# Kernel optimization log

Hardware: AMD Instinct MI355X
Metric: run time of the kernel (lower is better)

The kernel has to match this reference:

```python
import jax, jax.numpy as jnp
import numpy as np

N_HEADS = 16
NEG_INF = -10000.0


def setup_inputs() -> dict:
    key = jax.random.key(0)
    k1, k2, k3, k4 = jax.random.split(key, 4)
    B, S, D = 2, 2048, 1024
    q = jax.random.normal(k1, (B, S, D), dtype=jnp.float32)
    k = jax.random.normal(k2, (B, S, D), dtype=jnp.float32)
    v = jax.random.normal(k3, (B, S, D), dtype=jnp.float32)
    mask = jax.random.randint(k4, (B, S, S), 0, 2, dtype=jnp.int32)
    return {"q": q, "k": k, "v": v, "mask": mask}


def _mha(q, k, v, mask):
    B, S, D = q.shape
    H = N_HEADS
    hd = D // H
    # [B,S,D] -> [B,H,S,hd]
    qh = q.reshape(B, S, H, hd).transpose(0, 2, 1, 3)
    kh = k.reshape(B, S, H, hd).transpose(0, 2, 1, 3)
    vh = v.reshape(B, S, H, hd).transpose(0, 2, 1, 3)
    scores = jnp.einsum('bhqd,bhkd->bhqk', qh, kh) / jnp.sqrt(jnp.float32(hd))
    scores = scores + mask[:, None, :, :].astype(scores.dtype) * NEG_INF
    probs = jax.nn.softmax(scores, axis=-1)
    out = jnp.einsum('bhqk,bhkd->bhqd', probs, vh)
    return out.transpose(0, 2, 1, 3).reshape(B, S, D)


def reference(q, k, v, mask):
    return _mha(q, k, v, mask)
```

## Files before the change

kernel.cpp:

```cpp
#include <hip/hip_runtime.h>
#include <stdint.h>

#define S_LEN 2048
#define DMODEL 1024
#define NH 16
#define HD 64
#define NWORDS (S_LEN / 32)
#define NT (S_LEN / 64)

typedef __attribute__((ext_vector_type(4))) float f32x4;
typedef __attribute__((ext_vector_type(8))) short s16x8;
typedef __attribute__((ext_vector_type(4))) short s16x4;
typedef __attribute__((ext_vector_type(4))) int i32x4;
typedef __attribute__((ext_vector_type(2))) uint32_t u32x2;

__device__ __forceinline__ short f2bf(float x) {
  union { float f; uint32_t u; } v; v.f = x;
  return (short)((v.u + 0x8000u) >> 16);
}

__device__ __forceinline__ uint32_t cvtpk(float a, float b) {
  uint32_t r;
  asm("v_cvt_pk_bf16_f32 %0, %1, %2" : "=v"(r) : "v"(a), "v"(b));
  return r;
}

__device__ __forceinline__ float hexp2(float x) {
#if __has_builtin(__builtin_amdgcn_exp2f)
  return __builtin_amdgcn_exp2f(x);
#else
  float r;
  asm("v_exp_f32 %0, %1" : "=v"(r) : "v"(x));
  return r;
#endif
}

__device__ __forceinline__ f32x4 mfma32(s16x8 a, s16x8 b, f32x4 c) {
  return __builtin_amdgcn_mfma_f32_16x16x32_bf16(a, b, c, 0, 0, 0);
}

__device__ __forceinline__ f32x4 mfma16(s16x4 a, s16x4 b, f32x4 c) {
#if __has_builtin(__builtin_amdgcn_mfma_f32_16x16x16bf16_1k)
  return __builtin_amdgcn_mfma_f32_16x16x16bf16_1k(a, b, c, 0, 0, 0);
#else
  f32x4 d;
  asm("v_mfma_f32_16x16x16_bf16 %0, %1, %2, %3" : "=&v"(d) : "v"(a), "v"(b), "v"(c));
  return d;
#endif
}

typedef const __attribute__((address_space(1))) uint32_t* gas_u32p;
typedef __attribute__((address_space(3))) uint32_t* las_u32p;
__device__ __forceinline__ void gl_lds16(const void* g, void* l) {
  __builtin_amdgcn_global_load_lds((gas_u32p)g, (las_u32p)l, 16, 0, 0);
}

__global__ __launch_bounds__(256) void maskpack_kernel(
    const int* __restrict__ mask, uint32_t* __restrict__ bits, int ngroups) {
  const int lane = threadIdx.x & 63;
  const int wave = blockIdx.x * (blockDim.x >> 6) + (threadIdx.x >> 6);
  const int nw = gridDim.x * (blockDim.x >> 6);
  for (int gi = wave; gi < ngroups; gi += nw) {
    const int m = mask[(size_t)gi * 64 + lane];
    const unsigned long long bal = __ballot(m != 0);
    if (lane == 0) {
      bits[(size_t)gi * 2]     = (uint32_t)bal;
      bits[(size_t)gi * 2 + 1] = (uint32_t)(bal >> 32);
    }
  }
}

__global__ __launch_bounds__(256) void packkv_kernel(
    const float* __restrict__ k, const float* __restrict__ v,
    short* __restrict__ Kp, short* __restrict__ Vp) {
  const int t = blockIdx.x, h = blockIdx.y;
  const int b = blockIdx.z & 1, which = blockIdx.z >> 1;
  if (which == 0) {
    short* dst = Kp + (((size_t)(b * NH + h) * NT) + t) * 4096;
    const float* src0 = k + ((size_t)b * S_LEN + t * 64) * DMODEL + h * HD;
    for (int c = threadIdx.x; c < 512; c += 256) {
      const int kv = c >> 3, j = c & 7;
      const int jsrc = j ^ (kv & 7);
      const float* p = src0 + (size_t)kv * DMODEL + jsrc * 8;
      const f32x4 a = *(const f32x4*)p;
      const f32x4 bb = *(const f32x4*)(p + 4);
      s16x8 o;
      o[0]=f2bf(a[0]);  o[1]=f2bf(a[1]);  o[2]=f2bf(a[2]);  o[3]=f2bf(a[3]);
      o[4]=f2bf(bb[0]); o[5]=f2bf(bb[1]); o[6]=f2bf(bb[2]); o[7]=f2bf(bb[3]);
      *(s16x8*)(dst + (size_t)c * 8) = o;
    }
  } else {
    short* dst = Vp + (((size_t)(b * NH + h) * NT) + t) * 4096;
    const float* src0 = v + ((size_t)b * S_LEN + t * 64) * DMODEL + h * HD;
    for (int c = threadIdx.x; c < 1024; c += 256) {
      const int quad = c >> 6, dd = c & 63;
      const int d = dd ^ (quad & 7);
      const float* p = src0 + (size_t)quad * 4 * DMODEL + d;
      s16x4 o;
      o[0] = f2bf(p[0]);
      o[1] = f2bf(p[DMODEL]);
      o[2] = f2bf(p[2 * DMODEL]);
      o[3] = f2bf(p[3 * DMODEL]);
      *(s16x4*)(dst + (size_t)c * 4) = o;
    }
  }
}

__device__ __forceinline__ void tile_step7(
    int buf,
    const char*& kg, const char*& vg,
    const uint32_t*& bp0, const uint32_t*& bp1,
    char* klsb, char* vlsb, int so,
    int ka0, int ka1, int voE, int voO, int g4,
    const s16x8& qf00, const s16x8& qf01,
    const s16x8& qf10, const s16x8& qf11,
    u32x2& mwn0, u32x2& mwn1,
    f32x4 acc0[4], f32x4 acc1[4], f32x4& accs0, f32x4& accs1) {
  const f32x4 z4 = {0.f, 0.f, 0.f, 0.f};

  const u32x2 mw0 = mwn0, mw1 = mwn1;
  mwn0 = *(const u32x2*)bp0; bp0 += 2;
  mwn1 = *(const u32x2*)bp1; bp1 += 2;

  {
    char* kl = klsb + (buf ^ 1) * 8192 + so;
    char* vl = vlsb + (buf ^ 1) * 8192 + so;
    gl_lds16(kg, kl);  gl_lds16(kg + 1024, kl + 1024);
    gl_lds16(vg, vl);  gl_lds16(vg + 1024, vl + 1024);
    kg += 8192;
    vg += 8192;
  }

  f32x4 st0[4], st1[4];
  __builtin_amdgcn_s_setprio(1);
#pragma unroll
  for (int mi = 0; mi < 4; ++mi) {
    const char* rp = klsb + buf * 8192 + mi * 2048;
    const s16x8 kf0 = *(const s16x8*)(rp + ka0);
    const s16x8 kf1 = *(const s16x8*)(rp + ka1);
    st0[mi] = mfma32(kf1, qf01, mfma32(kf0, qf00, z4));
    st1[mi] = mfma32(kf1, qf11, mfma32(kf0, qf10, z4));
  }
  __builtin_amdgcn_s_setprio(0);

  const uint32_t wlo0 = mw0[0] >> g4, whi0 = mw0[1] >> g4;
  const uint32_t wlo1 = mw1[0] >> g4, whi1 = mw1[1] >> g4;
  s16x4 pf0[4], pf1[4];
#pragma unroll
  for (int mi = 0; mi < 4; ++mi) {
    const uint32_t w0 = (mi < 2) ? wlo0 : whi0;
    const uint32_t w1 = (mi < 2) ? wlo1 : whi1;
    const int bpos = (mi & 1) << 4;
    float p0[4], p1[4];
#pragma unroll
    for (int r = 0; r < 4; ++r) {
      union { float f; uint32_t u; } a, c;
      a.f = hexp2(st0[mi][r]);
      a.u &= (((w0 >> (bpos + r)) & 1u) - 1u);
      p0[r] = a.f;
      c.f = hexp2(st1[mi][r]);
      c.u &= (((w1 >> (bpos + r)) & 1u) - 1u);
      p1[r] = c.f;
    }
    union { uint32_t u[2]; s16x4 v4; } k0, k1;
    k0.u[0] = cvtpk(p0[0], p0[1]);  k0.u[1] = cvtpk(p0[2], p0[3]);
    k1.u[0] = cvtpk(p1[0], p1[1]);  k1.u[1] = cvtpk(p1[2], p1[3]);
    pf0[mi] = k0.v4;
    pf1[mi] = k1.v4;
  }

  const s16x4 onesb = {(short)0x3F80, (short)0x3F80, (short)0x3F80, (short)0x3F80};
  __builtin_amdgcn_s_setprio(1);
#pragma unroll
  for (int kc = 0; kc < 4; ++kc) {
    const char* vb = vlsb + buf * 8192 + kc * 2048;
    const int vo = (kc & 1) ? voO : voE;
    accs0 = mfma16(pf0[kc], onesb, accs0);
    accs1 = mfma16(pf1[kc], onesb, accs1);
#pragma unroll
    for (int dt = 0; dt < 4; ++dt) {
      const s16x4 vf = *(const s16x4*)(vb + dt * 128 + vo);
      acc0[dt] = mfma16(pf0[kc], vf, acc0[dt]);
      acc1[dt] = mfma16(pf1[kc], vf, acc1[dt]);
    }
  }
  __builtin_amdgcn_s_setprio(0);

  asm volatile("s_waitcnt vmcnt(0)" ::: "memory");
  __syncthreads();
}

__global__ __launch_bounds__(256, 2) void attn7_kernel(
    const float* __restrict__ q, const char* __restrict__ Kp,
    const char* __restrict__ Vp, const uint32_t* __restrict__ bits,
    float* __restrict__ out) {
  const int tid = threadIdx.x, lane = tid & 63, wid = tid >> 6;
  const int lq = lane & 15, g = lane >> 4, g4 = g << 2;

  const int wg = blockIdx.x;
  const int sz = ((wg & 7) << 6) | (wg >> 3);
  const int bx = sz & 15;
  const int h  = (sz >> 4) & 15;
  const int b  = sz >> 8;

  const int qbase = bx * 128 + wid * 32;
  const size_t bS = (size_t)b * S_LEN;
  const int qr0 = qbase + lq;
  const int qr1 = qbase + 16 + lq;

  __shared__ __align__(16) short kls[2][4096];
  __shared__ __align__(16) short vls[2][4096];

  const f32x4 z4 = {0.f, 0.f, 0.f, 0.f};
  const float SC = 0.125f * 1.44269504088896f;

  s16x8 qf00, qf01, qf10, qf11;
  {
    const float* qp = q + (bS + qr0) * (size_t)DMODEL + h * HD + g * 8;
    const f32x4 a0 = *(const f32x4*)qp;
    const f32x4 a1 = *(const f32x4*)(qp + 4);
    const f32x4 b0 = *(const f32x4*)(qp + 32);
    const f32x4 b1 = *(const f32x4*)(qp + 36);
    qf00[0]=f2bf(a0[0]*SC); qf00[1]=f2bf(a0[1]*SC);
    qf00[2]=f2bf(a0[2]*SC); qf00[3]=f2bf(a0[3]*SC);
    qf00[4]=f2bf(a1[0]*SC); qf00[5]=f2bf(a1[1]*SC);
    qf00[6]=f2bf(a1[2]*SC); qf00[7]=f2bf(a1[3]*SC);
    qf01[0]=f2bf(b0[0]*SC); qf01[1]=f2bf(b0[1]*SC);
    qf01[2]=f2bf(b0[2]*SC); qf01[3]=f2bf(b0[3]*SC);
    qf01[4]=f2bf(b1[0]*SC); qf01[5]=f2bf(b1[1]*SC);
    qf01[6]=f2bf(b1[2]*SC); qf01[7]=f2bf(b1[3]*SC);
  }
  {
    const float* qp = q + (bS + qr1) * (size_t)DMODEL + h * HD + g * 8;
    const f32x4 a0 = *(const f32x4*)qp;
    const f32x4 a1 = *(const f32x4*)(qp + 4);
    const f32x4 b0 = *(const f32x4*)(qp + 32);
    const f32x4 b1 = *(const f32x4*)(qp + 36);
    qf10[0]=f2bf(a0[0]*SC); qf10[1]=f2bf(a0[1]*SC);
    qf10[2]=f2bf(a0[2]*SC); qf10[3]=f2bf(a0[3]*SC);
    qf10[4]=f2bf(a1[0]*SC); qf10[5]=f2bf(a1[1]*SC);
    qf10[6]=f2bf(a1[2]*SC); qf10[7]=f2bf(a1[3]*SC);
    qf11[0]=f2bf(b0[0]*SC); qf11[1]=f2bf(b0[1]*SC);
    qf11[2]=f2bf(b0[2]*SC); qf11[3]=f2bf(b0[3]*SC);
    qf11[4]=f2bf(b1[0]*SC); qf11[5]=f2bf(b1[1]*SC);
    qf11[6]=f2bf(b1[2]*SC); qf11[7]=f2bf(b1[3]*SC);
  }

  const char* kg = Kp + ((size_t)(b * NH + h) * NT) * 8192 + wid * 2048 + lane * 16;
  const char* vg = Vp + ((size_t)(b * NH + h) * NT) * 8192 + wid * 2048 + lane * 16;
  const uint32_t* bp0 = bits + (bS + qr0) * NWORDS;
  const uint32_t* bp1 = bits + (bS + qr1) * NWORDS;

  f32x4 acc0[4] = {z4, z4, z4, z4};
  f32x4 acc1[4] = {z4, z4, z4, z4};
  f32x4 accs0 = z4, accs1 = z4;

  const int swk = (lq & 7) << 4;
  const int ka0 = lq * 128 + ((g * 16) ^ swk);
  const int ka1 = lq * 128 + ((64 + g * 16) ^ swk);
  const int voE = g * 512 + ((lq * 8) ^ (g * 8));
  const int voO = g * 512 + ((lq * 8) ^ (g * 8 + 32));
  const int so  = wid * 2048;

  u32x2 mwn0 = *(const u32x2*)bp0;  bp0 += 2;
  u32x2 mwn1 = *(const u32x2*)bp1;  bp1 += 2;

  {
    char* kl = (char*)kls + so;
    char* vl = (char*)vls + so;
    gl_lds16(kg, kl);  gl_lds16(kg + 1024, kl + 1024);
    gl_lds16(vg, vl);  gl_lds16(vg + 1024, vl + 1024);
    kg += 8192; vg += 8192;
  }
  asm volatile("s_waitcnt vmcnt(0)" ::: "memory");
  __syncthreads();

  for (int t2 = 0; t2 < NT; t2 += 2) {
    tile_step7(0, kg, vg, bp0, bp1, (char*)kls, (char*)vls, so,
               ka0, ka1, voE, voO, g4, qf00, qf01, qf10, qf11,
               mwn0, mwn1, acc0, acc1, accs0, accs1);
    tile_step7(1, kg, vg, bp0, bp1, (char*)kls, (char*)vls, so,
               ka0, ka1, voE, voO, g4, qf00, qf01, qf10, qf11,
               mwn0, mwn1, acc0, acc1, accs0, accs1);
  }

  float li0[4], li1[4];
#pragma unroll
  for (int r = 0; r < 4; ++r) {
    li0[r] = 1.0f / fmaxf(accs0[r], 1e-30f);
    li1[r] = 1.0f / fmaxf(accs1[r], 1e-30f);
  }
  float* ob0 = out + (bS + qbase) * (size_t)DMODEL + h * HD;
  float* ob1 = ob0 + (size_t)16 * DMODEL;
#pragma unroll
  for (int dt = 0; dt < 4; ++dt)
#pragma unroll
    for (int r = 0; r < 4; ++r) {
      ob0[(size_t)(g4 + r) * DMODEL + dt * 16 + lq] = acc0[dt][r] * li0[r];
      ob1[(size_t)(g4 + r) * DMODEL + dt * 16 + lq] = acc1[dt][r] * li1[r];
    }
}

template <int MASKBITS>
__global__ __launch_bounds__(256) void attn_kernel(
    const float* __restrict__ q, const float* __restrict__ k,
    const float* __restrict__ v, const int* __restrict__ mask,
    const uint32_t* __restrict__ bits, float* __restrict__ out) {
  const int tid  = threadIdx.x;
  const int lane = tid & 63;
  const int wid  = tid >> 6;
  const int lq   = lane & 15;
  const int g    = lane >> 4;
  const int g4   = g << 2;
  const int b    = blockIdx.z;
  const int h    = blockIdx.y;
  const int qw   = blockIdx.x * 128 + wid * 32;

  __shared__ __align__(16) short kls[64 * 64];
  __shared__ __align__(16) short vls[64 * 64];

  const size_t bS = (size_t)b * S_LEN;
  const float* qbase = q + bS * DMODEL + h * HD;
  const float* kbase = k + bS * DMODEL + h * HD;
  const float* vbase = v + bS * DMODEL + h * HD;

  const float LOG2E = 1.44269504088896f;
  const f32x4 z4 = {0.f, 0.f, 0.f, 0.f};

  s16x8 qf[2][2];
#pragma unroll
  for (int nq = 0; nq < 2; ++nq)
#pragma unroll
    for (int dc = 0; dc < 2; ++dc) {
      const float* p = qbase + (size_t)(qw + nq * 16 + lq) * DMODEL + dc * 32 + g * 8;
      const f32x4 a = *(const f32x4*)p;
      const f32x4 c = *(const f32x4*)(p + 4);
      s16x8 f;
      f[0] = f2bf(a[0] * 0.125f); f[1] = f2bf(a[1] * 0.125f);
      f[2] = f2bf(a[2] * 0.125f); f[3] = f2bf(a[3] * 0.125f);
      f[4] = f2bf(c[0] * 0.125f); f[5] = f2bf(c[1] * 0.125f);
      f[6] = f2bf(c[2] * 0.125f); f[7] = f2bf(c[3] * 0.125f);
      qf[nq][dc] = f;
    }

  f32x4 acc[2][4];
#pragma unroll
  for (int nq = 0; nq < 2; ++nq)
#pragma unroll
    for (int dt = 0; dt < 4; ++dt) acc[nq][dt] = z4;
  float mrun[2] = {-3.0e38f, -3.0e38f};
  float lrun[2] = {0.f, 0.f};

  const int kr  = tid >> 2;
  const int kc4 = (tid & 3) * 16;
  const int vq  = tid >> 4;
  const int vd  = (tid & 15) * 4;

  for (int t = 0; t < NT; ++t) {
    const int kvb = t * 64;
    uint32_t mw0[2], mw1[2];
    i32x4 mdir[2][4];
    if (MASKBITS) {
#pragma unroll
      for (int nq = 0; nq < 2; ++nq) {
        const uint32_t* bpp = bits + (bS + qw + nq * 16 + lq) * NWORDS + (kvb >> 5);
        const u32x2 w = *(const u32x2*)bpp;
        mw0[nq] = w[0]; mw1[nq] = w[1];
      }
    } else {
#pragma unroll
      for (int nq = 0; nq < 2; ++nq)
#pragma unroll
        for (int mi = 0; mi < 4; ++mi)
          mdir[nq][mi] = *(const i32x4*)(mask + (bS + qw + nq * 16 + lq) * S_LEN +
                                         kvb + mi * 16 + g4);
    }

    __syncthreads();
    {
      const float* p = kbase + (size_t)(kvb + kr) * DMODEL + kc4;
      const f32x4 x0 = *(const f32x4*)p;
      const f32x4 x1 = *(const f32x4*)(p + 4);
      const f32x4 x2 = *(const f32x4*)(p + 8);
      const f32x4 x3 = *(const f32x4*)(p + 12);
      s16x8 lo, hi;
      lo[0]=f2bf(x0[0]); lo[1]=f2bf(x0[1]); lo[2]=f2bf(x0[2]); lo[3]=f2bf(x0[3]);
      lo[4]=f2bf(x1[0]); lo[5]=f2bf(x1[1]); lo[6]=f2bf(x1[2]); lo[7]=f2bf(x1[3]);
      hi[0]=f2bf(x2[0]); hi[1]=f2bf(x2[1]); hi[2]=f2bf(x2[2]); hi[3]=f2bf(x2[3]);
      hi[4]=f2bf(x3[0]); hi[5]=f2bf(x3[1]); hi[6]=f2bf(x3[2]); hi[7]=f2bf(x3[3]);
      char* rowp = (char*)kls + kr * 128;
      const int sw2 = (kr & 7) << 4;
      *(s16x8*)(rowp + ((kc4 * 2) ^ sw2))      = lo;
      *(s16x8*)(rowp + ((kc4 * 2 + 16) ^ sw2)) = hi;
    }
    {
      const float* p = vbase + (size_t)(kvb + vq * 4) * DMODEL + vd;
      const f32x4 r0 = *(const f32x4*)p;
      const f32x4 r1 = *(const f32x4*)(p + DMODEL);
      const f32x4 r2 = *(const f32x4*)(p + 2 * DMODEL);
      const f32x4 r3 = *(const f32x4*)(p + 3 * DMODEL);
      char* rowp = (char*)vls + vq * 512;
      const int sw2 = (vq & 7) << 3;
#pragma unroll
      for (int j = 0; j < 4; ++j) {
        s16x4 pk;
        pk[0] = f2bf(r0[j]); pk[1] = f2bf(r1[j]);
        pk[2] = f2bf(r2[j]); pk[3] = f2bf(r3[j]);
        *(s16x4*)(rowp + (((vd + j) * 8) ^ sw2)) = pk;
      }
    }
    __syncthreads();

    f32x4 stv[2][4];
#pragma unroll
    for (int mi = 0; mi < 4; ++mi) {
      const char* rp = (const char*)kls + (mi * 16 + lq) * 128;
      const int sw2 = (lq & 7) << 4;
      const s16x8 kf0 = *(const s16x8*)(rp + ((g * 16) ^ sw2));
      const s16x8 kf1 = *(const s16x8*)(rp + ((64 + g * 16) ^ sw2));
      stv[0][mi] = mfma32(kf0, qf[0][0], z4);
      stv[0][mi] = mfma32(kf1, qf[0][1], stv[0][mi]);
      stv[1][mi] = mfma32(kf0, qf[1][0], z4);
      stv[1][mi] = mfma32(kf1, qf[1][1], stv[1][mi]);
    }

    s16x4 pf[2][4];
#pragma unroll
    for (int nq = 0; nq < 2; ++nq) {
#pragma unroll
      for (int mi = 0; mi < 4; ++mi) {
#pragma unroll
        for (int r = 0; r < 4; ++r) {
          float mz;
          if (MASKBITS) {
            const uint32_t w = (mi < 2) ? mw0[nq] : mw1[nq];
            const int sh = ((mi & 1) << 4) + g4 + r;
            mz = (float)((w >> sh) & 1u);
          } else {
            mz = (float)mdir[nq][mi][r];
          }
          stv[nq][mi][r] = stv[nq][mi][r] - 10000.0f * mz;
        }
      }
      float mx = -3.0e38f;
#pragma unroll
      for (int mi = 0; mi < 4; ++mi)
#pragma unroll
        for (int r = 0; r < 4; ++r) mx = fmaxf(mx, stv[nq][mi][r]);
      mx = fmaxf(mx, __shfl_xor(mx, 16));
      mx = fmaxf(mx, __shfl_xor(mx, 32));
      const float mnew = fmaxf(mrun[nq], mx);
      const float al = exp2f((mrun[nq] - mnew) * LOG2E);
      mrun[nq] = mnew;
      const float nms = mnew * LOG2E;
      float sum = 0.f;
#pragma unroll
      for (int mi = 0; mi < 4; ++mi)
#pragma unroll
        for (int r = 0; r < 4; ++r) {
          const float p = exp2f(__builtin_fmaf(stv[nq][mi][r], LOG2E, -nms));
          stv[nq][mi][r] = p;
          sum += p;
        }
      sum += __shfl_xor(sum, 16);
      sum += __shfl_xor(sum, 32);
      lrun[nq] = lrun[nq] * al + sum;
      float aO[4];
#pragma unroll
      for (int r = 0; r < 4; ++r) aO[r] = __shfl(al, g4 + r);
#pragma unroll
      for (int dt = 0; dt < 4; ++dt)
#pragma unroll
        for (int r = 0; r < 4; ++r) acc[nq][dt][r] *= aO[r];
#pragma unroll
      for (int kc = 0; kc < 4; ++kc) {
        s16x4 pp;
#pragma unroll
        for (int r = 0; r < 4; ++r) pp[r] = f2bf(stv[nq][kc][r]);
        pf[nq][kc] = pp;
      }
    }

#pragma unroll
    for (int kc = 0; kc < 4; ++kc) {
#pragma unroll
      for (int dt = 0; dt < 4; ++dt) {
        const int quad = kc * 4 + g;
        const s16x4 vf = *(const s16x4*)((const char*)vls + quad * 512 +
                                         (((dt * 16 + lq) * 8) ^ ((quad & 7) << 3)));
        acc[0][dt] = mfma16(pf[0][kc], vf, acc[0][dt]);
        acc[1][dt] = mfma16(pf[1][kc], vf, acc[1][dt]);
      }
    }
  }

  float* obase = out + bS * DMODEL + h * HD;
#pragma unroll
  for (int nq = 0; nq < 2; ++nq) {
    const float linv = 1.0f / lrun[nq];
    float li[4];
#pragma unroll
    for (int r = 0; r < 4; ++r) li[r] = __shfl(linv, g4 + r);
#pragma unroll
    for (int dt = 0; dt < 4; ++dt)
#pragma unroll
      for (int r = 0; r < 4; ++r)
        obase[(size_t)(qw + nq * 16 + g4 + r) * DMODEL + dt * 16 + lq] =
            acc[nq][dt][r] * li[r];
  }
}

extern "C" void kernel_launch(void* const* d_in, const int* in_sizes, int n_in,
                              void* d_out, int out_size, void* d_ws, size_t ws_size,
                              hipStream_t stream) {
  const float* q   = (const float*)d_in[0];
  const float* k   = (const float*)d_in[1];
  const float* v   = (const float*)d_in[2];
  const int* mask  = (const int*)d_in[3];
  float* out       = (float*)d_out;

  const size_t bits_bytes = (size_t)2 * S_LEN * NWORDS * sizeof(uint32_t);
  const size_t pack_bytes = (size_t)2 * S_LEN * DMODEL * sizeof(short);
  const size_t full_bytes = bits_bytes + 2 * pack_bytes + 16384;

  if (ws_size >= full_bytes) {
    char* w = (char*)d_ws;
    uint32_t* bits = (uint32_t*)w;
    char* Kp = w + bits_bytes;
    char* Vp = w + bits_bytes + pack_bytes;

    const int ngroups = 2 * S_LEN * (S_LEN / 64);
    maskpack_kernel<<<512, 256, 0, stream>>>(mask, bits, ngroups);
    packkv_kernel<<<dim3(NT, NH, 4), 256, 0, stream>>>(k, v, (short*)Kp, (short*)Vp);
    attn7_kernel<<<512, 256, 0, stream>>>(q, Kp, Vp, bits, out);
  } else if (ws_size >= bits_bytes) {
    uint32_t* bits = (uint32_t*)d_ws;
    const int ngroups = 2 * S_LEN * (S_LEN / 64);
    maskpack_kernel<<<512, 256, 0, stream>>>(mask, bits, ngroups);
    attn_kernel<1><<<dim3(S_LEN / 128, NH, 2), 256, 0, stream>>>(
        q, k, v, mask, bits, out);
  } else {
    attn_kernel<0><<<dim3(S_LEN / 128, NH, 2), 256, 0, stream>>>(
        q, k, v, mask, nullptr, out);
  }
}
```

Measured before the change: 93.55 us.

## Split KV sequence across two wave groups per block with LDS reduction

Doubles the block to 512 threads, with two groups of four waves each handling half of the key/value tiles (16 tiles each) for the same 128 query rows. Each group has its own double-buffered K/V LDS region. Partial output and row-sum accumulators are then combined through shared memory before normalization and store. This aims to shorten the serial KV loop per block and raise the number of waves in flight. The cost is more LDS per block (64KB), an extra reduction and barrier, and possible occupancy limits at 512 threads.

Result: no change. 95.25 us (+1.8%).

```diff
diff --git a/kernel.cpp b/kernel.cpp
--- a/kernel.cpp
+++ b/kernel.cpp
@@ -190,11 +190,12 @@
   __syncthreads();
 }
 
-__global__ __launch_bounds__(256, 2) void attn7_kernel(
+__global__ __launch_bounds__(512, 2) void attn8_kernel(
     const float* __restrict__ q, const char* __restrict__ Kp,
     const char* __restrict__ Vp, const uint32_t* __restrict__ bits,
     float* __restrict__ out) {
   const int tid = threadIdx.x, lane = tid & 63, wid = tid >> 6;
+  const int qw4 = wid & 3, ks = wid >> 2;
   const int lq = lane & 15, g = lane >> 4, g4 = g << 2;
 
   const int wg = blockIdx.x;
@@ -203,13 +204,14 @@
   const int h  = (sz >> 4) & 15;
   const int b  = sz >> 8;
 
-  const int qbase = bx * 128 + wid * 32;
+  const int qbase = bx * 128 + qw4 * 32;
   const size_t bS = (size_t)b * S_LEN;
   const int qr0 = qbase + lq;
   const int qr1 = qbase + 16 + lq;
 
-  __shared__ __align__(16) short kls[2][4096];
-  __shared__ __align__(16) short vls[2][4096];
+  __shared__ __align__(16) char smem[65536];
+  char* klsb = smem + ks * 16384;
+  char* vlsb = smem + 32768 + ks * 16384;
 
   const f32x4 z4 = {0.f, 0.f, 0.f, 0.f};
   const float SC = 0.125f * 1.44269504088896f;
@@ -246,10 +248,12 @@
     qf11[6]=f2bf(b1[2]*SC); qf11[7]=f2bf(b1[3]*SC);
   }
 
-  const char* kg = Kp + ((size_t)(b * NH + h) * NT) * 8192 + wid * 2048 + lane * 16;
-  const char* vg = Vp + ((size_t)(b * NH + h) * NT) * 8192 + wid * 2048 + lane * 16;
-  const uint32_t* bp0 = bits + (bS + qr0) * NWORDS;
-  const uint32_t* bp1 = bits + (bS + qr1) * NWORDS;
+  const char* kg = Kp + ((size_t)(b * NH + h) * NT + ks * 16) * 8192 +
+                   qw4 * 2048 + lane * 16;
+  const char* vg = Vp + ((size_t)(b * NH + h) * NT + ks * 16) * 8192 +
+                   qw4 * 2048 + lane * 16;
+  const uint32_t* bp0 = bits + (bS + qr0) * NWORDS + ks * 32;
+  const uint32_t* bp1 = bits + (bS + qr1) * NWORDS + ks * 32;
 
   f32x4 acc0[4] = {z4, z4, z4, z4};
   f32x4 acc1[4] = {z4, z4, z4, z4};
@@ -260,14 +264,14 @@
   const int ka1 = lq * 128 + ((64 + g * 16) ^ swk);
   const int voE = g * 512 + ((lq * 8) ^ (g * 8));
   const int voO = g * 512 + ((lq * 8) ^ (g * 8 + 32));
-  const int so  = wid * 2048;
+  const int so  = qw4 * 2048;
 
   u32x2 mwn0 = *(const u32x2*)bp0;  bp0 += 2;
   u32x2 mwn1 = *(const u32x2*)bp1;  bp1 += 2;
 
   {
-    char* kl = (char*)kls + so;
-    char* vl = (char*)vls + so;
+    char* kl = klsb + so;
+    char* vl = vlsb + so;
     gl_lds16(kg, kl);  gl_lds16(kg + 1024, kl + 1024);
     gl_lds16(vg, vl);  gl_lds16(vg + 1024, vl + 1024);
     kg += 8192; vg += 8192;
@@ -275,30 +279,53 @@
   asm volatile("s_waitcnt vmcnt(0)" ::: "memory");
   __syncthreads();
 
-  for (int t2 = 0; t2 < NT; t2 += 2) {
-    tile_step7(0, kg, vg, bp0, bp1, (char*)kls, (char*)vls, so,
+  for (int t2 = 0; t2 < 16; t2 += 2) {
+    tile_step7(0, kg, vg, bp0, bp1, klsb, vlsb, so,
                ka0, ka1, voE, voO, g4, qf00, qf01, qf10, qf11,
                mwn0, mwn1, acc0, acc1, accs0, accs1);
-    tile_step7(1, kg, vg, bp0, bp1, (char*)kls, (char*)vls, so,
+    tile_step7(1, kg, vg, bp0, bp1, klsb, vlsb, so,
                ka0, ka1, voE, voO, g4, qf00, qf01, qf10, qf11,
                mwn0, mwn1, acc0, acc1, accs0, accs1);
   }
 
-  float li0[4], li1[4];
-#pragma unroll
-  for (int r = 0; r < 4; ++r) {
-    li0[r] = 1.0f / fmaxf(accs0[r], 1e-30f);
-    li1[r] = 1.0f / fmaxf(accs1[r], 1e-30f);
-  }
-  float* ob0 = out + (bS + qbase) * (size_t)DMODEL + h * HD;
-  float* ob1 = ob0 + (size_t)16 * DMODEL;
-#pragma unroll
-  for (int dt = 0; dt < 4; ++dt)
+  float* red = (float*)smem;
+  if (ks == 1) {
+    float* rp = red + (size_t)(qw4 * 64 + lane) * 44;
+#pragma unroll
+    for (int dt = 0; dt < 4; ++dt) {
+      *(f32x4*)(rp + 4 * dt)      = acc0[dt];
+      *(f32x4*)(rp + 16 + 4 * dt) = acc1[dt];
+    }
+    *(f32x4*)(rp + 32) = accs0;
+    *(f32x4*)(rp + 36) = accs1;
+  }
+  __syncthreads();
+  if (ks == 0) {
+    const float* rp = red + (size_t)(qw4 * 64 + lane) * 44;
+#pragma unroll
+    for (int dt = 0; dt < 4; ++dt) {
+      acc0[dt] += *(const f32x4*)(rp + 4 * dt);
+      acc1[dt] += *(const f32x4*)(rp + 16 + 4 * dt);
+    }
+    accs0 += *(const f32x4*)(rp + 32);
+    accs1 += *(const f32x4*)(rp + 36);
+
+    float li0[4], li1[4];
 #pragma unroll
     for (int r = 0; r < 4; ++r) {
-      ob0[(size_t)(g4 + r) * DMODEL + dt * 16 + lq] = acc0[dt][r] * li0[r];
-      ob1[(size_t)(g4 + r) * DMODEL + dt * 16 + lq] = acc1[dt][r] * li1[r];
-    }
+      li0[r] = 1.0f / fmaxf(accs0[r], 1e-30f);
+      li1[r] = 1.0f / fmaxf(accs1[r], 1e-30f);
+    }
+    float* ob0 = out + (bS + qbase) * (size_t)DMODEL + h * HD;
+    float* ob1 = ob0 + (size_t)16 * DMODEL;
+#pragma unroll
+    for (int dt = 0; dt < 4; ++dt)
+#pragma unroll
+      for (int r = 0; r < 4; ++r) {
+        ob0[(size_t)(g4 + r) * DMODEL + dt * 16 + lq] = acc0[dt][r] * li0[r];
+        ob1[(size_t)(g4 + r) * DMODEL + dt * 16 + lq] = acc1[dt][r] * li1[r];
+      }
+  }
 }
 
 template <int MASKBITS>
@@ -532,7 +559,7 @@
     const int ngroups = 2 * S_LEN * (S_LEN / 64);
     maskpack_kernel<<<512, 256, 0, stream>>>(mask, bits, ngroups);
     packkv_kernel<<<dim3(NT, NH, 4), 256, 0, stream>>>(k, v, (short*)Kp, (short*)Vp);
-    attn7_kernel<<<512, 256, 0, stream>>>(q, Kp, Vp, bits, out);
+    attn8_kernel<<<512, 512, 0, stream>>>(q, Kp, Vp, bits, out);
   } else if (ws_size >= bits_bytes) {
     uint32_t* bits = (uint32_t*)d_ws;
     const int ngroups = 2 * S_LEN * (S_LEN / 64);
```
